# Performance work log

Measured on AMD Instinct MI355X. Metric: run time of the kernel, lower is better.

## Reference

```python
import jax, jax.numpy as jnp
import numpy as np
from jax import lax

C, CMID, RED, SCALE, KUP, KENC = 128, 64, 8, 2, 5, 3


def _conv(x, w, b=None, pad=0, groups=1):
    y = lax.conv_general_dilated(x, w, (1, 1), [(pad, pad), (pad, pad)],
                                 feature_group_count=groups,
                                 dimension_numbers=('NCHW', 'OIHW', 'NCHW'))
    if b is not None:
        y = y + b[None, :, None, None]
    return y


def setup_inputs() -> dict:
    key = jax.random.key(0)
    ks = jax.random.split(key, 8)
    s = 0.05
    return {
        'X': jax.random.normal(ks[0], (2, C, 64, 64), jnp.float32),
        'w3': jax.random.normal(ks[1], (CMID, C, 3, 3), jnp.float32) * s,
        'b3': jnp.zeros((CMID,), jnp.float32),
        'w5': jax.random.normal(ks[2], (CMID, C, 5, 5), jnp.float32) * s,
        'b5': jnp.zeros((CMID,), jnp.float32),
        'wa1': jax.random.normal(ks[3], (CMID // RED, CMID, 1, 1), jnp.float32) * s,
        'ba1': jnp.zeros((CMID // RED,), jnp.float32),
        'wa2': jax.random.normal(ks[4], (CMID, CMID // RED, 1, 1), jnp.float32) * s,
        'ba2': jnp.zeros((CMID,), jnp.float32),
        'wedge': jax.random.normal(ks[5], (CMID, 1, 3, 3), jnp.float32) * s,
        'wenc': jax.random.normal(ks[6], ((SCALE * KUP) ** 2, CMID, KENC, KENC), jnp.float32) * s,
    }


def reference(X, w3, b3, w5, b5, wa1, ba1, wa2, ba2, wedge, wenc):
    b, c, h, w = X.shape
    h_, w_ = h * SCALE, w * SCALE

    # kernel-prediction branch: 3x3 + 5x5 compression convs
    W = _conv(X, w3, b3, pad=1) + _conv(X, w5, b5, pad=2)

    # DetailEnhanceAttention: SE-style channel gate + depthwise edge conv
    avg = jnp.mean(W, axis=(2, 3), keepdims=True)            # (b, cmid, 1, 1)
    a = _conv(avg, wa1, ba1, pad=0)
    a = jax.nn.sigmoid(_conv(a, wa2, ba2, pad=0))
    edge = _conv(W, wedge, None, pad=1, groups=CMID)          # depthwise 3x3
    W = W * a + edge

    # encoder conv -> (b, (scale*k_up)^2, h, w)
    W = _conv(W, wenc, None, pad=KENC // 2)

    # PixelShuffle(scale): channels (k_up^2, r, r) -> (k_up^2, h*r, w*r)
    Wp = W.reshape(b, KUP * KUP, SCALE, SCALE, h, w)
    Wp = Wp.transpose(0, 1, 4, 2, 5, 3).reshape(b, KUP * KUP, h_, w_)
    Wp = jax.nn.softmax(Wp, axis=1)                           # softmax over k_up^2 taps

    # nearest upsample of X to (b, c, h_, w_)
    Xu = jnp.repeat(jnp.repeat(X, SCALE, axis=2), SCALE, axis=3)

    # unfold: kernel=k_up, dilation=scale, padding=k_up//2*scale
    p = (KUP // 2) * SCALE
    Xpad = jnp.pad(Xu, ((0, 0), (0, 0), (p, p), (p, p)))
    # (b, c, k_up^2, h_, w_), tap index = ki*k_up + kj (torch unfold order)
    patches = jnp.stack([
        Xpad[:, :, i * SCALE:i * SCALE + h_, j * SCALE:j * SCALE + w_]
        for i in range(KUP) for j in range(KUP)
    ], axis=2)

    out = jnp.einsum('bkhw,bckhw->bchw', Wp, patches)
    return out
```

## Files before the change

kernel.cpp:

```cpp
#include <hip/hip_runtime.h>
#include <math.h>

typedef __attribute__((ext_vector_type(2))) _Float16 f16x2;
typedef __attribute__((ext_vector_type(4))) _Float16 f16x4;
typedef __attribute__((ext_vector_type(8))) _Float16 f16x8;
typedef __attribute__((ext_vector_type(4))) float f32x4;

#if __has_builtin(__builtin_amdgcn_fdot2)
#define FDOT2(a, b, c) __builtin_amdgcn_fdot2((a), (b), (c), false)
#else
static __device__ __forceinline__ float FDOT2(f16x2 a, f16x2 b, float c) {
  return c + (float)a[0] * (float)b[0] + (float)a[1] * (float)b[1];
}
#endif

#define XPAD8_B  0
#define WFC_B    2506752
#define WFE_B    2916352
#define WFEATP_B 3045376
#define WEDGET_B 4194304
#define BCOMB_B  4195456
#define AVG_B    4195712

__global__ __launch_bounds__(256) void prep_kernel(
    const float* __restrict__ X,
    const float* __restrict__ w3, const float* __restrict__ b3,
    const float* __restrict__ w5, const float* __restrict__ b5,
    const float* __restrict__ wedge, const float* __restrict__ wenc,
    char* __restrict__ wsb) {
  int idx = blockIdx.x * 256 + threadIdx.x;
  if (idx < 156672) {
    int x = idx % 72;
    int t = idx / 72;
    int y = t % 68;
    int t2 = t / 68;
    int gg = t2 & 15, b = t2 >> 4;
    int yy = y - 2, xx = x - 2;
    bool ok = (yy >= 0 && yy < 64 && xx >= 0 && xx < 64);
    f16x8 h;
#pragma unroll
    for (int j = 0; j < 8; ++j) {
      float v = ok ? X[((b * 128 + gg * 8 + j) << 12) + yy * 64 + xx] : 0.f;
      h[j] = (_Float16)v;
    }
    ((f16x8*)(wsb + XPAD8_B))[idx] = h;
  }
  if (idx < 25600) {
    int l = idx & 63;
    int q = idx >> 6;
    int ntg = q & 3;
    int q2 = q >> 2;
    int cc = q2 & 3;
    int t = q2 >> 2;
    int ky = t / 5, kx = t % 5;
    int oc = ntg * 16 + (l & 15);
    int ci0 = cc * 32 + (l >> 4) * 8;
    f16x8 h;
#pragma unroll
    for (int i = 0; i < 8; ++i) {
      int ci = ci0 + i;
      float v = w5[(oc * 128 + ci) * 25 + t];
      if (ky >= 1 && ky <= 3 && kx >= 1 && kx <= 3)
        v += w3[(oc * 128 + ci) * 9 + (ky - 1) * 3 + (kx - 1)];
      h[i] = (_Float16)v;
    }
    ((f16x8*)(wsb + WFC_B))[idx] = h;
  }
  if (idx < 8064) {
    int l = idx & 63;
    int q = idx >> 6;
    int nt = q % 7;
    int q2 = q / 7;
    int cc = q2 & 1;
    int t = q2 >> 1;
    int oc = nt * 16 + (l & 15);
    int ci0 = cc * 32 + (l >> 4) * 8;
    f16x8 h;
#pragma unroll
    for (int i = 0; i < 8; ++i) {
      float v = (oc < 100) ? wenc[(oc * 64 + ci0 + i) * 9 + t] : 0.f;
      h[i] = (_Float16)v;
    }
    ((f16x8*)(wsb + WFE_B))[idx] = h;
  }
  if (idx < 6272) {
    int plane = idx / 392, p = idx % 392;
    int r, c;
    if (p < 136) {
      r = (p >= 68) ? 65 : 0;
      c = p % 68;
    } else {
      int q = p - 136;
      r = 1 + (q >> 2);
      int cm = q & 3;
      c = (cm == 0) ? 0 : (64 + cm);
    }
    f16x8 z = {(_Float16)0.f, (_Float16)0.f, (_Float16)0.f, (_Float16)0.f,
               (_Float16)0.f, (_Float16)0.f, (_Float16)0.f, (_Float16)0.f};
    *(f16x8*)((_Float16*)(wsb + WFEATP_B) + ((size_t)(plane * 66 + r) * 68 + c) * 8) = z;
  }
  if (idx < 72) {
    int k = idx >> 3, gg = idx & 7;
    f16x8 h;
#pragma unroll
    for (int j = 0; j < 8; ++j) h[j] = (_Float16)wedge[(gg * 8 + j) * 9 + k];
    ((f16x8*)(wsb + WEDGET_B))[idx] = h;
  }
  if (idx < 64) ((float*)(wsb + BCOMB_B))[idx] = b3[idx] + b5[idx];
  if (idx < 128) ((float*)(wsb + AVG_B))[idx] = b3[idx & 63] + b5[idx & 63];
}

__global__ __launch_bounds__(256) void convw_kernel(
    const _Float16* __restrict__ xpad8, const f16x8* __restrict__ wfc,
    const float* __restrict__ bcomb, _Float16* __restrict__ wfeatp,
    float* __restrict__ avg) {
  __shared__ __attribute__((aligned(16))) _Float16 xs[16 * 776];
  __shared__ float red[2][64][4];
  __shared__ float redm[2][16];
  const int tid = threadIdx.x;
  const int z = blockIdx.z;
  const int b = z >> 2, ntg = z & 3;
  const int tx0 = blockIdx.x * 8, ty0 = blockIdx.y * 4;

  for (int u = tid; u < 1536; u += 256) {
    int gg = u / 96;
    int rem = u - gg * 96;
    int r = rem / 12, c = rem - r * 12;
    f16x8 v = *(const f16x8*)&xpad8[((size_t)((b * 16 + gg) * 68 + ty0 + r) * 72 + tx0 + c) * 8];
    *(f16x8*)&xs[gg * 776 + r * 96 + c * 8] = v;
  }
  __syncthreads();

  const int w = __builtin_amdgcn_readfirstlane(tid >> 6);
  const int l = tid & 63;
  const int pg = w & 1, kh = w >> 1;
  const int lm = l & 15, lg = l >> 4;
  const int p = pg * 16 + lm;
  const int abase = (p >> 3) * 96 + (p & 7) * 8;

  f32x4 acc = {0.f, 0.f, 0.f, 0.f};
  for (int dy = 0; dy < 5; ++dy) {
    for (int dx = 0; dx < 5; ++dx) {
      const int t = dy * 5 + dx;
      const int toff = abase + dy * 96 + dx * 8;
#pragma unroll
      for (int cc2 = 0; cc2 < 2; ++cc2) {
        const int cc = kh * 2 + cc2;
        f16x8 a = *(const f16x8*)&xs[(cc * 4 + lg) * 776 + toff];
        f16x8 bb = wfc[((t * 4 + cc) * 4 + ntg) * 64 + l];
        acc = __builtin_amdgcn_mfma_f32_16x16x32_f16(a, bb, acc, 0, 0, 0);
      }
    }
  }

  if (kh == 1) {
#pragma unroll
    for (int r = 0; r < 4; ++r) red[pg][l][r] = acc[r];
  }
  __syncthreads();
  if (kh == 0) {
#pragma unroll
    for (int r = 0; r < 4; ++r) acc[r] += red[pg][l][r];
    float s = acc[0] + acc[1] + acc[2] + acc[3];
    s += __shfl_xor(s, 16);
    s += __shfl_xor(s, 32);
    if (lg == 0) redm[pg][lm] = s;
    const float bias = bcomb[ntg * 16 + lm];
#pragma unroll
    for (int r = 0; r < 4; ++r) {
      int pd = pg * 16 + lg * 4 + r;
      xs[pd * 24 + lm] = (_Float16)(acc[r] + bias);
    }
  }
  __syncthreads();
  if (tid < 64) {
    int pd = tid >> 1, g2 = tid & 1;
    f16x8 v = *(const f16x8*)&xs[pd * 24 + g2 * 8];
    int gy = ty0 + (pd >> 3), gx = tx0 + (pd & 7);
    *(f16x8*)&wfeatp[((size_t)((b * 8 + ntg * 2 + g2) * 66 + 1 + gy) * 68 + 1 + gx) * 8] = v;
  }
  if (tid < 16) {
    float tot = redm[0][tid] + redm[1][tid];
    atomicAdd(&avg[b * 64 + ntg * 16 + tid], tot * (1.f / 4096.f));
  }
}

#define SM_XT  0
#define SM_XSV 9984
#define SM_TS  15232
#define SM_SML 15232
#define SM_SMW 22656
#define SM_WED 26496
#define SM_TLA 27648
#define SM_GSH 27680
#define SM_TOT 27936

__global__ __launch_bounds__(256) void enccarafe_kernel(
    const _Float16* __restrict__ wfeatp, const f16x8* __restrict__ wfe,
    const _Float16* __restrict__ xpad8, const f16x8* __restrict__ wedgeT,
    const float* __restrict__ wa1, const float* __restrict__ ba1,
    const float* __restrict__ wa2, const float* __restrict__ ba2,
    const float* __restrict__ avg, float* __restrict__ out) {
  __shared__ __attribute__((aligned(16))) char smem[SM_TOT];
  _Float16* xt = (_Float16*)(smem + SM_XT);
  _Float16* xsv = (_Float16*)(smem + SM_XSV);
  _Float16* ts = (_Float16*)(smem + SM_TS);
  float* sml = (float*)(smem + SM_SML);
  f16x2* smw2 = (f16x2*)(smem + SM_SMW);
  f16x8* wedt = (f16x8*)(smem + SM_WED);
  float* tlat = (float*)(smem + SM_TLA);
  float* gsh = (float*)(smem + SM_GSH);

  const int tid = threadIdx.x;
  const int z = blockIdx.z;
  const int b = z >> 1, cq = z & 1;
  const int tx0 = blockIdx.x * 8, ty0 = blockIdx.y * 2;

  for (int u = tid; u < 624; u += 256) {
    int gg = u / 78;
    int rem = u - gg * 78;
    int r = rem / 13, c = rem - r * 13;
    f16x8 v = *(const f16x8*)&xpad8[((size_t)((b * 16 + cq * 8 + gg) * 68 + ty0 + r) * 72 + tx0 + c) * 8];
    *(f16x8*)&xt[gg * 624 + r * 104 + c * 8] = v;
  }
  for (int u = tid; u < 576; u += 256) {
    int gg = u / 72;
    int rem = u - gg * 72;
    int r = rem / 12, c = rem - r * 12;
    int pr = ty0 - 1 + r, pc = tx0 - 1 + c;
    f16x8 v = {(_Float16)0.f, (_Float16)0.f, (_Float16)0.f, (_Float16)0.f,
               (_Float16)0.f, (_Float16)0.f, (_Float16)0.f, (_Float16)0.f};
    if (pr >= 0 && pr < 66 && pc >= 0 && pc < 68)
      v = *(const f16x8*)&wfeatp[((size_t)((b * 8 + gg) * 66 + pr) * 68 + pc) * 8];
    *(f16x8*)&ts[gg * 584 + r * 96 + c * 8] = v;
  }
  if (tid < 72) wedt[tid] = wedgeT[tid];
  if (tid < 8) {
    float s = ba1[tid];
    for (int i = 0; i < 64; ++i) s += wa1[tid * 64 + i] * avg[b * 64 + i];
    tlat[tid] = s;
  }
  __syncthreads();
  if (tid < 64) {
    float s = ba2[tid];
#pragma unroll
    for (int j = 0; j < 8; ++j) s += wa2[tid * 8 + j] * tlat[j];
    gsh[tid] = 1.f / (1.f + expf(-s));
  }
  __syncthreads();

  for (int u = tid; u < 320; u += 256) {
    int gg = u / 40;
    int rem = u - gg * 40;
    int r6 = rem / 10, c10 = rem - r6 * 10;
    int vy = ty0 - 1 + r6, vx = tx0 - 1 + c10;
    f16x8 res = {(_Float16)0.f, (_Float16)0.f, (_Float16)0.f, (_Float16)0.f,
                 (_Float16)0.f, (_Float16)0.f, (_Float16)0.f, (_Float16)0.f};
    if (vy >= 0 && vy < 64 && vx >= 0 && vx < 64) {
      float vout[8];
      f16x8 ctr = *(const f16x8*)&ts[gg * 584 + (r6 + 1) * 96 + (c10 + 1) * 8];
#pragma unroll
      for (int j = 0; j < 8; ++j) vout[j] = (float)ctr[j] * gsh[gg * 8 + j];
#pragma unroll
      for (int ky = 0; ky < 3; ++ky) {
#pragma unroll
        for (int kx = 0; kx < 3; ++kx) {
          int k = ky * 3 + kx;
          f16x8 tv = *(const f16x8*)&ts[gg * 584 + (r6 + ky) * 96 + (c10 + kx) * 8];
          f16x8 wv = wedt[k * 8 + gg];
#pragma unroll
          for (int j = 0; j < 8; ++j) vout[j] = fmaf((float)wv[j], (float)tv[j], vout[j]);
        }
      }
#pragma unroll
      for (int j = 0; j < 8; ++j) res[j] = (_Float16)vout[j];
    }
    *(f16x8*)&xsv[gg * 328 + r6 * 80 + c10 * 8] = res;
  }
  __syncthreads();

  {
    const int w = __builtin_amdgcn_readfirstlane(tid >> 6);
    const int l = tid & 63;
    const int lm = l & 15, lg = l >> 4;
    const int abase = (lm >> 3) * 80 + (lm & 7) * 8;
    const int nt0 = w * 2;
    const int ncnt = (w == 3) ? 1 : 2;

    f32x4 a0 = {0.f, 0.f, 0.f, 0.f}, a1 = {0.f, 0.f, 0.f, 0.f};
    for (int dy = 0; dy < 3; ++dy) {
      for (int dx = 0; dx < 3; ++dx) {
        const int t = dy * 3 + dx;
        const int toff = abase + dy * 80 + dx * 8;
#pragma unroll
        for (int cc = 0; cc < 2; ++cc) {
          f16x8 a = *(const f16x8*)&xsv[(cc * 4 + lg) * 328 + toff];
          f16x8 b0 = wfe[((t * 2 + cc) * 7 + nt0) * 64 + l];
          a0 = __builtin_amdgcn_mfma_f32_16x16x32_f16(a, b0, a0, 0, 0, 0);
          if (ncnt == 2) {
            f16x8 b1 = wfe[((t * 2 + cc) * 7 + nt0 + 1) * 64 + l];
            a1 = __builtin_amdgcn_mfma_f32_16x16x32_f16(a, b1, a1, 0, 0, 0);
          }
        }
      }
    }
#pragma unroll
    for (int r = 0; r < 4; ++r) {
      sml[(4 * lg + r) * 116 + nt0 * 16 + lm] = a0[r];
      if (ncnt == 2) sml[(4 * lg + r) * 116 + (nt0 + 1) * 16 + lm] = a1[r];
    }
  }
  __syncthreads();

  if (tid < 64) {
    int pix = tid >> 2, sub = tid & 3;
    float lv[25];
    float m = -1e30f;
#pragma unroll
    for (int k = 0; k < 25; ++k) {
      lv[k] = sml[pix * 116 + k * 4 + sub];
      m = fmaxf(m, lv[k]);
    }
    float s = 0.f;
#pragma unroll
    for (int k = 0; k < 25; ++k) {
      lv[k] = __expf(lv[k] - m);
      s += lv[k];
    }
    float inv = 1.f / s;
#pragma unroll
    for (int ki = 0; ki < 5; ++ki) {
#pragma unroll
      for (int pr = 0; pr < 3; ++pr) {
        float wlo = lv[ki * 5 + 2 * pr] * inv;
        float whi = (2 * pr + 1 < 5) ? lv[ki * 5 + 2 * pr + 1] * inv : 0.f;
        f16x2 pk = {(_Float16)wlo, (_Float16)whi};
        smw2[((ki * 3 + pr) * 16 + pix) * 4 + sub] = pk;
      }
    }
  }
  __syncthreads();

  {
    const int slot = tid >> 5;
    const int rem = tid & 31;
    const int syh = rem >> 4, pix = rem & 15;
    const int py = pix >> 3, px = pix & 7;
    const _Float16* xb = xt + slot * 624;

    float acc[2][8];
#pragma unroll
    for (int s = 0; s < 2; ++s)
#pragma unroll
      for (int j = 0; j < 8; ++j) acc[s][j] = 0.f;

    union U8 { f16x8 v; unsigned int u[4]; };
#pragma unroll
    for (int ki = 0; ki < 5; ++ki) {
      const _Float16* row = xb + (py + ki) * 104 + px * 8;
      U8 C[6];
#pragma unroll
      for (int c = 0; c < 6; ++c) C[c].v = *(const f16x8*)(row + c * 8);
#pragma unroll
      for (int pr = 0; pr < 3; ++pr) {
        const f16x2* wp = &smw2[((ki * 3 + pr) * 16 + pix) * 4 + syh * 2];
        f16x2 w0 = wp[0], w1 = wp[1];
        const U8& A = C[2 * pr];
        const U8& B = C[2 * pr + 1];
#pragma unroll
        for (int k = 0; k < 4; ++k) {
          unsigned int lo = __builtin_amdgcn_perm(B.u[k], A.u[k], 0x05040100u);
          unsigned int hi = __builtin_amdgcn_perm(B.u[k], A.u[k], 0x07060302u);
          f16x2 xlo = __builtin_bit_cast(f16x2, lo);
          f16x2 xhi = __builtin_bit_cast(f16x2, hi);
          acc[0][2 * k] = FDOT2(w0, xlo, acc[0][2 * k]);
          acc[1][2 * k] = FDOT2(w1, xlo, acc[1][2 * k]);
          acc[0][2 * k + 1] = FDOT2(w0, xhi, acc[0][2 * k + 1]);
          acc[1][2 * k + 1] = FDOT2(w1, xhi, acc[1][2 * k + 1]);
        }
      }
    }
    int y0o = 2 * (ty0 + py) + syh, x0o = 2 * (tx0 + px);
#pragma unroll
    for (int j = 0; j < 8; ++j) {
      int c = cq * 64 + slot * 8 + j;
      float* op = out + ((size_t)(b * 128 + c) * 128 + y0o) * 128 + x0o;
      float2 v0 = {acc[0][j], acc[1][j]};
      *(float2*)op = v0;
    }
  }
}

extern "C" void kernel_launch(void* const* d_in, const int* in_sizes, int n_in,
                              void* d_out, int out_size, void* d_ws, size_t ws_size,
                              hipStream_t stream) {
  const float* X     = (const float*)d_in[0];
  const float* w3    = (const float*)d_in[1];
  const float* b3    = (const float*)d_in[2];
  const float* w5    = (const float*)d_in[3];
  const float* b5    = (const float*)d_in[4];
  const float* wa1   = (const float*)d_in[5];
  const float* ba1   = (const float*)d_in[6];
  const float* wa2   = (const float*)d_in[7];
  const float* ba2   = (const float*)d_in[8];
  const float* wedge = (const float*)d_in[9];
  const float* wenc  = (const float*)d_in[10];
  char* wsb = (char*)d_ws;
  float* out = (float*)d_out;

  _Float16* xpad8  = (_Float16*)(wsb + XPAD8_B);
  f16x8*    wfc    = (f16x8*)(wsb + WFC_B);
  f16x8*    wfe    = (f16x8*)(wsb + WFE_B);
  _Float16* wfeatp = (_Float16*)(wsb + WFEATP_B);
  f16x8*    wedgeT = (f16x8*)(wsb + WEDGET_B);
  float*    bcomb  = (float*)(wsb + BCOMB_B);
  float*    avg    = (float*)(wsb + AVG_B);

  prep_kernel<<<612, 256, 0, stream>>>(X, w3, b3, w5, b5, wedge, wenc, wsb);
  convw_kernel<<<dim3(8, 16, 8), 256, 0, stream>>>(xpad8, wfc, bcomb, wfeatp, avg);
  enccarafe_kernel<<<dim3(8, 32, 4), 256, 0, stream>>>(
      wfeatp, wfe, xpad8, wedgeT, wa1, ba1, wa2, ba2, avg, out);
}
```

Baseline: 49.96 us.

## Retile encoder-CARAFE kernel to 4x2 pixel tiles covering all channels per block

Each enccarafe block previously covered an 8x2 pixel tile for half of the 128 output channels, so the two channel halves each recomputed the edge conv, the encoder MFMA conv and the softmax. Blocks now cover a 4x2 pixel tile for all 128 channels, which removes that duplicated per-pixel work and loads the wfeatp halo once per tile. The cost is larger relative halos per pixel and half-empty MFMA tiles, since only 8 of the 16 rows are valid pixels.

Result: slower. 52.53 us (+5.1%).

```diff
diff --git a/kernel.cpp b/kernel.cpp
--- a/kernel.cpp
+++ b/kernel.cpp
@@ -185,15 +185,18 @@
   }
 }
 
+#define GS_XT  440
+#define GS_TS  440
+#define GS_XSV 232
 #define SM_XT  0
-#define SM_XSV 9984
-#define SM_TS  15232
-#define SM_SML 15232
-#define SM_SMW 22656
-#define SM_WED 26496
-#define SM_TLA 27648
-#define SM_GSH 27680
-#define SM_TOT 27936
+#define SM_XSV 14080
+#define SM_TS  17792
+#define SM_SML 17792
+#define SM_SMW 21504
+#define SM_WED 24832
+#define SM_TLA 25984
+#define SM_GSH 26016
+#define SM_TOT 26272
 
 __global__ __launch_bounds__(256) void enccarafe_kernel(
     const _Float16* __restrict__ wfeatp, const f16x8* __restrict__ wfe,
@@ -212,27 +215,26 @@
   float* gsh = (float*)(smem + SM_GSH);
 
   const int tid = threadIdx.x;
-  const int z = blockIdx.z;
-  const int b = z >> 1, cq = z & 1;
-  const int tx0 = blockIdx.x * 8, ty0 = blockIdx.y * 2;
-
-  for (int u = tid; u < 624; u += 256) {
-    int gg = u / 78;
-    int rem = u - gg * 78;
-    int r = rem / 13, c = rem - r * 13;
-    f16x8 v = *(const f16x8*)&xpad8[((size_t)((b * 16 + cq * 8 + gg) * 68 + ty0 + r) * 72 + tx0 + c) * 8];
-    *(f16x8*)&xt[gg * 624 + r * 104 + c * 8] = v;
-  }
-  for (int u = tid; u < 576; u += 256) {
-    int gg = u / 72;
-    int rem = u - gg * 72;
-    int r = rem / 12, c = rem - r * 12;
+  const int b = blockIdx.z;
+  const int tx0 = blockIdx.x * 4, ty0 = blockIdx.y * 2;
+
+  for (int u = tid; u < 864; u += 256) {
+    int gg = u / 54;
+    int rem = u - gg * 54;
+    int r = rem / 9, c = rem - r * 9;
+    f16x8 v = *(const f16x8*)&xpad8[((size_t)((b * 16 + gg) * 68 + ty0 + r) * 72 + tx0 + c) * 8];
+    *(f16x8*)&xt[gg * GS_XT + r * 72 + c * 8] = v;
+  }
+  for (int u = tid; u < 384; u += 256) {
+    int gg = u / 48;
+    int rem = u - gg * 48;
+    int r = rem / 8, c = rem - r * 8;
     int pr = ty0 - 1 + r, pc = tx0 - 1 + c;
     f16x8 v = {(_Float16)0.f, (_Float16)0.f, (_Float16)0.f, (_Float16)0.f,
                (_Float16)0.f, (_Float16)0.f, (_Float16)0.f, (_Float16)0.f};
     if (pr >= 0 && pr < 66 && pc >= 0 && pc < 68)
       v = *(const f16x8*)&wfeatp[((size_t)((b * 8 + gg) * 66 + pr) * 68 + pc) * 8];
-    *(f16x8*)&ts[gg * 584 + r * 96 + c * 8] = v;
+    *(f16x8*)&ts[gg * GS_TS + r * 72 + c * 8] = v;
   }
   if (tid < 72) wedt[tid] = wedgeT[tid];
   if (tid < 8) {
@@ -249,16 +251,16 @@
   }
   __syncthreads();
 
-  for (int u = tid; u < 320; u += 256) {
-    int gg = u / 40;
-    int rem = u - gg * 40;
-    int r6 = rem / 10, c10 = rem - r6 * 10;
-    int vy = ty0 - 1 + r6, vx = tx0 - 1 + c10;
+  if (tid < 192) {
+    int gg = tid / 24;
+    int rem = tid - gg * 24;
+    int r4 = rem / 6, c6 = rem - r4 * 6;
+    int vy = ty0 - 1 + r4, vx = tx0 - 1 + c6;
     f16x8 res = {(_Float16)0.f, (_Float16)0.f, (_Float16)0.f, (_Float16)0.f,
                  (_Float16)0.f, (_Float16)0.f, (_Float16)0.f, (_Float16)0.f};
     if (vy >= 0 && vy < 64 && vx >= 0 && vx < 64) {
       float vout[8];
-      f16x8 ctr = *(const f16x8*)&ts[gg * 584 + (r6 + 1) * 96 + (c10 + 1) * 8];
+      f16x8 ctr = *(const f16x8*)&ts[gg * GS_TS + (r4 + 1) * 72 + (c6 + 1) * 8];
 #pragma unroll
       for (int j = 0; j < 8; ++j) vout[j] = (float)ctr[j] * gsh[gg * 8 + j];
 #pragma unroll
@@ -266,7 +268,7 @@
 #pragma unroll
         for (int kx = 0; kx < 3; ++kx) {
           int k = ky * 3 + kx;
-          f16x8 tv = *(const f16x8*)&ts[gg * 584 + (r6 + ky) * 96 + (c10 + kx) * 8];
+          f16x8 tv = *(const f16x8*)&ts[gg * GS_TS + (r4 + ky) * 72 + (c6 + kx) * 8];
           f16x8 wv = wedt[k * 8 + gg];
 #pragma unroll
           for (int j = 0; j < 8; ++j) vout[j] = fmaf((float)wv[j], (float)tv[j], vout[j]);
@@ -275,7 +277,7 @@
 #pragma unroll
       for (int j = 0; j < 8; ++j) res[j] = (_Float16)vout[j];
     }
-    *(f16x8*)&xsv[gg * 328 + r6 * 80 + c10 * 8] = res;
+    *(f16x8*)&xsv[gg * GS_XSV + r4 * 56 + c6 * 8] = res;
   }
   __syncthreads();
 
@@ -283,7 +285,8 @@
     const int w = __builtin_amdgcn_readfirstlane(tid >> 6);
     const int l = tid & 63;
     const int lm = l & 15, lg = l >> 4;
-    const int abase = (lm >> 3) * 80 + (lm & 7) * 8;
+    const int px4 = lm & 3, py2 = (lm >> 2) & 1;
+    const int abase = py2 * 56 + px4 * 8;
     const int nt0 = w * 2;
     const int ncnt = (w == 3) ? 1 : 2;
 
@@ -291,10 +294,10 @@
     for (int dy = 0; dy < 3; ++dy) {
       for (int dx = 0; dx < 3; ++dx) {
         const int t = dy * 3 + dx;
-        const int toff = abase + dy * 80 + dx * 8;
+        const int toff = abase + dy * 56 + dx * 8;
 #pragma unroll
         for (int cc = 0; cc < 2; ++cc) {
-          f16x8 a = *(const f16x8*)&xsv[(cc * 4 + lg) * 328 + toff];
+          f16x8 a = *(const f16x8*)&xsv[(cc * 4 + lg) * GS_XSV + toff];
           f16x8 b0 = wfe[((t * 2 + cc) * 7 + nt0) * 64 + l];
           a0 = __builtin_amdgcn_mfma_f32_16x16x32_f16(a, b0, a0, 0, 0, 0);
           if (ncnt == 2) {
@@ -306,13 +309,16 @@
     }
 #pragma unroll
     for (int r = 0; r < 4; ++r) {
-      sml[(4 * lg + r) * 116 + nt0 * 16 + lm] = a0[r];
-      if (ncnt == 2) sml[(4 * lg + r) * 116 + (nt0 + 1) * 16 + lm] = a1[r];
-    }
-  }
-  __syncthreads();
-
-  if (tid < 64) {
+      int pd = 4 * lg + r;
+      if (pd < 8) {
+        sml[pd * 116 + nt0 * 16 + lm] = a0[r];
+        if (ncnt == 2) sml[pd * 116 + (nt0 + 1) * 16 + lm] = a1[r];
+      }
+    }
+  }
+  __syncthreads();
+
+  if (tid < 32) {
     int pix = tid >> 2, sub = tid & 3;
     float lv[25];
     float m = -1e30f;
@@ -335,18 +341,18 @@
         float wlo = lv[ki * 5 + 2 * pr] * inv;
         float whi = (2 * pr + 1 < 5) ? lv[ki * 5 + 2 * pr + 1] * inv : 0.f;
         f16x2 pk = {(_Float16)wlo, (_Float16)whi};
-        smw2[((ki * 3 + pr) * 16 + pix) * 4 + sub] = pk;
+        smw2[((ki * 3 + pr) * 8 + pix) * 4 + sub] = pk;
       }
     }
   }
   __syncthreads();
 
   {
-    const int slot = tid >> 5;
-    const int rem = tid & 31;
-    const int syh = rem >> 4, pix = rem & 15;
-    const int py = pix >> 3, px = pix & 7;
-    const _Float16* xb = xt + slot * 624;
+    const int slot = tid >> 4;
+    const int rem = tid & 15;
+    const int syh = rem >> 3, pix = rem & 7;
+    const int py = pix >> 2, px = pix & 3;
+    const _Float16* xb = xt + slot * GS_XT;
 
     float acc[2][8];
 #pragma unroll
@@ -357,13 +363,13 @@
     union U8 { f16x8 v; unsigned int u[4]; };
 #pragma unroll
     for (int ki = 0; ki < 5; ++ki) {
-      const _Float16* row = xb + (py + ki) * 104 + px * 8;
+      const _Float16* row = xb + (py + ki) * 72 + px * 8;
       U8 C[6];
 #pragma unroll
       for (int c = 0; c < 6; ++c) C[c].v = *(const f16x8*)(row + c * 8);
 #pragma unroll
       for (int pr = 0; pr < 3; ++pr) {
-        const f16x2* wp = &smw2[((ki * 3 + pr) * 16 + pix) * 4 + syh * 2];
+        const f16x2* wp = &smw2[((ki * 3 + pr) * 8 + pix) * 4 + syh * 2];
         f16x2 w0 = wp[0], w1 = wp[1];
         const U8& A = C[2 * pr];
         const U8& B = C[2 * pr + 1];
@@ -383,7 +389,7 @@
     int y0o = 2 * (ty0 + py) + syh, x0o = 2 * (tx0 + px);
 #pragma unroll
     for (int j = 0; j < 8; ++j) {
-      int c = cq * 64 + slot * 8 + j;
+      int c = slot * 8 + j;
       float* op = out + ((size_t)(b * 128 + c) * 128 + y0o) * 128 + x0o;
       float2 v0 = {acc[0][j], acc[1][j]};
       *(float2*)op = v0;
@@ -418,6 +424,6 @@
 
   prep_kernel<<<612, 256, 0, stream>>>(X, w3, b3, w5, b5, wedge, wenc, wsb);
   convw_kernel<<<dim3(8, 16, 8), 256, 0, stream>>>(xpad8, wfc, bcomb, wfeatp, avg);
-  enccarafe_kernel<<<dim3(8, 32, 4), 256, 0, stream>>>(
+  enccarafe_kernel<<<dim3(16, 32, 2), 256, 0, stream>>>(
       wfeatp, wfe, xpad8, wedgeT, wa1, ba1, wa2, ba2, avg, out);
 }
```
